# Optimization experiments

Measured on AMD Instinct MI355X. Metric: run time of the kernel, lower is better.

Reference implementation:

```python
import jax, jax.numpy as jnp
import numpy as np

T, B, D, H = 256, 64, 1024, 1024


def setup_inputs() -> dict:
    key = jax.random.key(0)
    ks = jax.random.split(key, 12)
    stdv = 1.0 / np.sqrt(H)
    u = lambda k, shape: jax.random.uniform(k, shape, jnp.float32, -stdv, stdv)
    return {
        "input_": jax.random.normal(ks[0], (T, B, D), jnp.float32),
        "length": jax.random.randint(ks[1], (B,), 1, T + 1, jnp.int32),
        "h0": jnp.zeros((B, H), jnp.float32),
        "cj": jax.random.normal(ks[2], (B, H), jnp.float32),
        "he": jax.random.normal(ks[3], (B, H), jnp.float32),
        "w_ih": u(ks[4], (3 * H, D)),
        "w_hh": u(ks[5], (3 * H, H)),
        "w_ch": u(ks[6], (3 * H, H)),
        "w_zh": u(ks[7], (3 * H, H)),
        "b_ih": u(ks[8], (3 * H,)),
        "b_hh": u(ks[9], (3 * H,)),
        "b_ch": u(ks[10], (3 * H,)),
        "b_zh": u(ks[11], (3 * H,)),
    }


def _chunk3(g):
    # mirrors torch .chunk(3, 1) on a (..., 3H) tensor
    return g[..., :H], g[..., H:2 * H], g[..., 2 * H:]


def reference(input_, length, h0, cj, he, w_ih, w_hh, w_ch, w_zh,
              b_ih, b_hh, b_ch, b_zh):
    # context projections are time-invariant: hoist out of the recurrence
    c_r, c_i, c_n = _chunk3(cj @ w_ch.T + b_ch)   # (B,H) each
    z_r, z_i, z_n = _chunk3(he @ w_zh.T + b_zh)   # (B,H) each
    # input projections for all steps at once: (T,B,3H)
    gi_all = jnp.einsum('tbd,gd->tbg', input_, w_ih) + b_ih

    def step(h, xs):
        gi_t, t = xs
        i_r, i_i, i_n = _chunk3(gi_t)
        h_r, h_i, h_n_ = _chunk3(h @ w_hh.T + b_hh)
        resetgate = jax.nn.sigmoid(i_r + h_r + c_r + z_r)
        inputgate = jax.nn.sigmoid(i_i + h_i + c_i + z_i)
        newgate = jnp.tanh(i_n + resetgate * h_n_ + c_n + z_n)
        hy = newgate + inputgate * (h - newgate)
        mask = (t < length).astype(hy.dtype)[:, None]          # (B,1)
        # NOTE: faithful to original torch code, which uses hx[0]
        # (first batch row, broadcast) in the masked branch.
        h_next = hy * mask + h[0] * (1.0 - mask)
        return h_next, h_next

    h_last, output = jax.lax.scan(step, h0, (gi_all, jnp.arange(T)))
    h_n = h_last[None]  # (num_layers=1, B, H)
    return output, h_n
```

## Files before the change

### kernel.cpp

```cpp
#include <hip/hip_runtime.h>
#include <stdint.h>

#define TT 256
#define BB 64
#define DD 1024
#define HH 1024
#define G3 3072

typedef unsigned long long ull;
typedef __attribute__((ext_vector_type(8))) short short8;
typedef __attribute__((ext_vector_type(4))) float f32x4;

__device__ __forceinline__ unsigned short f2bf(float f) {
  union { float f; unsigned int i; } v; v.f = f;
  unsigned int x = v.i;
  return (unsigned short)((x + 0x7fffu + ((x >> 16) & 1u)) >> 16);
}
__device__ __forceinline__ float bf2f(unsigned short u) {
  union { unsigned int i; float f; } v; v.i = ((unsigned int)u) << 16; return v.f;
}
__device__ __forceinline__ f32x4 mfma16(short8 a, short8 b, f32x4 c) {
  return __builtin_amdgcn_mfma_f32_16x16x32_bf16(a, b, c, 0, 0, 0);
}
__device__ __forceinline__ void gload_lds16(const void* g, void* l) {
  __builtin_amdgcn_global_load_lds((const __attribute__((address_space(1))) void*)g,
                                   (__attribute__((address_space(3))) void*)l,
                                   16, 0, 0);
}

__global__ void k_cvt_bf16(const float* __restrict__ in, unsigned short* __restrict__ out, int n4) {
  int i = blockIdx.x * blockDim.x + threadIdx.x;
  int stride = gridDim.x * blockDim.x;
  for (; i < n4; i += stride) {
    float4 v = ((const float4*)in)[i];
    ushort4 o;
    o.x = f2bf(v.x); o.y = f2bf(v.y); o.z = f2bf(v.z); o.w = f2bf(v.w);
    ((ushort4*)out)[i] = o;
  }
}

__global__ __launch_bounds__(256) void k_ctx(
    const unsigned short* __restrict__ cjb, const unsigned short* __restrict__ heb,
    const unsigned short* __restrict__ Wchb, const unsigned short* __restrict__ Wzhb,
    const float* __restrict__ b_ih, const float* __restrict__ b_hh,
    const float* __restrict__ b_ch, const float* __restrict__ b_zh,
    float* __restrict__ E) {
  __shared__ f32x4 red[4][4][64];
  int n0 = blockIdx.x * 16;
  int tid = threadIdx.x;
  int w = tid >> 6, l = tid & 63, lo = l & 15, hi = l >> 4;
  f32x4 acc[4];
#pragma unroll
  for (int r = 0; r < 4; r++) acc[r] = (f32x4){0.f, 0.f, 0.f, 0.f};
#pragma unroll 4
  for (int kk = 0; kk < 16; kk++) {
    int k = w * 512 + kk * 32;
    const unsigned short* Asrc = (k < 1024) ? cjb : heb;
    const unsigned short* Bsrc = (k < 1024) ? Wchb : Wzhb;
    int kw = (k < 1024) ? k : (k - 1024);
    int kof = kw + hi * 8;
    short8 bf = *(const short8*)(Bsrc + (size_t)(n0 + lo) * 1024 + kof);
#pragma unroll
    for (int r = 0; r < 4; r++) {
      short8 af = *(const short8*)(Asrc + (size_t)(r * 16 + lo) * 1024 + kof);
      acc[r] = mfma16(af, bf, acc[r]);
    }
  }
#pragma unroll
  for (int r = 0; r < 4; r++) red[w][r][l] = acc[r];
  __syncthreads();
  f32x4 s = red[0][w][l];
#pragma unroll
  for (int w2 = 1; w2 < 4; w2++) {
    f32x4 p = red[w2][w][l];
    s[0] += p[0]; s[1] += p[1]; s[2] += p[2]; s[3] += p[3];
  }
  int g = n0 + lo;
  float bias = b_ih[g] + b_ch[g] + b_zh[g] + ((g < 2048) ? b_hh[g] : 0.0f);
#pragma unroll
  for (int j = 0; j < 4; j++) {
    int b = w * 16 + hi * 4 + j;
    E[(size_t)b * G3 + g] = s[j] + bias;
  }
}

__global__ __launch_bounds__(256) void k_gemm_gi(
    const unsigned short* __restrict__ Xb,
    const unsigned short* __restrict__ Wb,
    const float* __restrict__ E,
    unsigned short* __restrict__ gi) {
  __shared__ unsigned short As[128 * 32];
  __shared__ unsigned short Bs[128 * 32];
  int bid = blockIdx.x;
  int mt = bid & 127;
  int nt = bid >> 7;
  int m0 = mt * 128, n0 = nt * 128;
  int tid = threadIdx.x;
  int w = tid >> 6, l = tid & 63, lo = l & 15, hi = l >> 4;
  int wr = w >> 1, wc = w & 1;
  f32x4 acc[4][4];
#pragma unroll
  for (int i = 0; i < 4; i++)
#pragma unroll
    for (int j = 0; j < 4; j++) acc[i][j] = (f32x4){0.f, 0.f, 0.f, 0.f};
  int srow = tid >> 2;
  int scol = (tid & 3) * 8;
  for (int kt = 0; kt < 32; kt++) {
    int k0 = kt * 32;
    __syncthreads();
    gload_lds16(Xb + (size_t)(m0 + srow) * 1024 + k0 + scol, As + srow * 32 + scol);
    gload_lds16(Xb + (size_t)(m0 + 64 + srow) * 1024 + k0 + scol, As + (64 + srow) * 32 + scol);
    gload_lds16(Wb + (size_t)(n0 + srow) * 1024 + k0 + scol, Bs + srow * 32 + scol);
    gload_lds16(Wb + (size_t)(n0 + 64 + srow) * 1024 + k0 + scol, Bs + (64 + srow) * 32 + scol);
    asm volatile("s_waitcnt vmcnt(0)" ::: "memory");
    __syncthreads();
    short8 a[4], b[4];
#pragma unroll
    for (int i = 0; i < 4; i++) a[i] = *(const short8*)(As + (wr * 64 + i * 16 + lo) * 32 + hi * 8);
#pragma unroll
    for (int i = 0; i < 4; i++) b[i] = *(const short8*)(Bs + (wc * 64 + i * 16 + lo) * 32 + hi * 8);
#pragma unroll
    for (int i = 0; i < 4; i++)
#pragma unroll
      for (int j = 0; j < 4; j++) acc[i][j] = mfma16(a[i], b[j], acc[i][j]);
  }
#pragma unroll
  for (int i = 0; i < 4; i++)
#pragma unroll
    for (int j = 0; j < 4; j++)
#pragma unroll
      for (int e = 0; e < 4; e++) {
        int r = m0 + wr * 64 + i * 16 + hi * 4 + e;
        int c = n0 + wc * 64 + j * 16 + lo;
        float v = acc[i][j][e] + E[(size_t)(r & 63) * G3 + c];
        gi[(size_t)r * G3 + c] = f2bf(v);
      }
}

__global__ __launch_bounds__(256) void k_rnn(
    const unsigned short* __restrict__ giE,
    const unsigned short* __restrict__ Whhb,
    const float* __restrict__ b_hh,
    const float* __restrict__ h0,
    const int* __restrict__ length,
    unsigned short* __restrict__ hbuf,
    float* __restrict__ out,
    float* __restrict__ hn,
    unsigned int* __restrict__ seq) {
  extern __shared__ char smem[];
  unsigned short* wlds = (unsigned short*)smem;
  f32x4* red = (f32x4*)(smem + 98304);
  float* hp0 = (float*)(smem + 98304 + 49152);

  const int cs = blockIdx.x;
  const int j0 = cs * 16;
  const int tid = threadIdx.x;
  const int kq = tid >> 6, l = tid & 63, lo = l & 15, hi = l >> 4;
  const int rowbase = kq * 16;
  const int col = j0 + lo;

#pragma unroll
  for (int kk = 0; kk < 8; ++kk)
#pragma unroll
    for (int s = 0; s < 3; ++s) {
      int f = (kq * 8 + kk) * 3 + s;
      short8 v = *(const short8*)(Whhb + (size_t)(s * 1024 + j0 + lo) * 1024 + kq * 256 + kk * 32 + hi * 8);
      ((short8*)wlds)[f * 64 + l] = v;
    }

  const float bhhn = b_hh[2048 + col];
  float hown[4];
  int len4[4];
#pragma unroll
  for (int j = 0; j < 4; ++j) {
    int b = rowbase + hi * 4 + j;
    hown[j] = h0[(size_t)b * 1024 + col];
    len4[j] = length[b];
  }
#pragma unroll
  for (int j = 0; j < 4; ++j) {
    unsigned int mine = f2bf(hown[j]);
    unsigned int oth = __shfl_xor(mine, 1, 64);
    if (!(lo & 1)) {
      int row = rowbase + hi * 4 + j;
      __hip_atomic_store((unsigned int*)(hbuf + (size_t)cs * 1024 + row * 16 + lo),
                         mine | (oth << 16), __ATOMIC_RELAXED, __HIP_MEMORY_SCOPE_AGENT);
    }
  }
  if (kq == 0 && hi == 0) hp0[lo] = hown[0];
  float gir[3][4];
#pragma unroll
  for (int s = 0; s < 3; ++s)
#pragma unroll
    for (int j = 0; j < 4; ++j)
      gir[s][j] = bf2f(giE[(size_t)(rowbase + hi * 4 + j) * G3 + s * 1024 + col]);
  __syncthreads();
  asm volatile("s_waitcnt vmcnt(0)" ::: "memory");
  if (l == 0)
    __hip_atomic_store(&seq[(cs * 4 + kq) * 16], 1u, __ATOMIC_RELAXED, __HIP_MEMORY_SCOPE_AGENT);

  int slot = 0;
  for (int t = 0; t < TT; ++t) {
    const int nslot = (slot == 2) ? 0 : slot + 1;
    {
      const unsigned int* sp = seq + ((size_t)(kq * 16 + (l >> 2)) * 4 + (l & 3)) * 16;
      unsigned int tgt = (unsigned int)(t + 1);
      for (;;) {
        unsigned int v = __hip_atomic_load(sp, __ATOMIC_RELAXED, __HIP_MEMORY_SCOPE_AGENT);
        if (__all(v >= tgt)) break;
        __builtin_amdgcn_s_sleep(1);
      }
    }
    const unsigned short* hb2 = hbuf + (size_t)slot * 65536;
    union AF { ull u[2]; short8 v; };
    AF a[4][8];
#pragma unroll
    for (int rt = 0; rt < 4; ++rt)
#pragma unroll
      for (int kk = 0; kk < 8; ++kk) {
        int k = kq * 256 + kk * 32;
        int blk = (k >> 4) + (hi >> 1);
        const unsigned short* hp = hb2 + (size_t)blk * 1024 + (rt * 16 + lo) * 16 + (hi & 1) * 8;
        a[rt][kk].u[0] = __hip_atomic_load((const ull*)hp, __ATOMIC_RELAXED, __HIP_MEMORY_SCOPE_AGENT);
        a[rt][kk].u[1] = __hip_atomic_load((const ull*)hp + 1, __ATOMIC_RELAXED, __HIP_MEMORY_SCOPE_AGENT);
      }
    f32x4 acc[4][3];
#pragma unroll
    for (int rt = 0; rt < 4; ++rt)
#pragma unroll
      for (int s = 0; s < 3; ++s) acc[rt][s] = (f32x4){0.f, 0.f, 0.f, 0.f};
#pragma unroll
    for (int kk = 0; kk < 8; ++kk) {
      const short8* wf = ((const short8*)wlds) + (size_t)((kq * 8 + kk) * 3) * 64 + l;
      short8 b0 = wf[0];
      short8 b1 = wf[64];
      short8 b2 = wf[128];
#pragma unroll
      for (int rt = 0; rt < 4; ++rt) {
        acc[rt][0] = mfma16(a[rt][kk].v, b0, acc[rt][0]);
        acc[rt][1] = mfma16(a[rt][kk].v, b1, acc[rt][1]);
        acc[rt][2] = mfma16(a[rt][kk].v, b2, acc[rt][2]);
      }
    }
#pragma unroll
    for (int rt = 0; rt < 4; ++rt)
#pragma unroll
      for (int s = 0; s < 3; ++s)
        red[((size_t)kq * 12 + rt * 3 + s) * 64 + l] = acc[rt][s];
    __syncthreads();
    f32x4 fin[3];
#pragma unroll
    for (int s = 0; s < 3; ++s) {
      f32x4 v = red[((size_t)0 * 12 + kq * 3 + s) * 64 + l];
#pragma unroll
      for (int q = 1; q < 4; ++q) {
        f32x4 p = red[((size_t)q * 12 + kq * 3 + s) * 64 + l];
        v[0] += p[0]; v[1] += p[1]; v[2] += p[2]; v[3] += p[3];
      }
      fin[s] = v;
    }
    float h0p = hp0[(t & 1) * 16 + lo];
    __syncthreads();
    float hv[4];
#pragma unroll
    for (int j = 0; j < 4; ++j) {
      float R = fin[0][j] + gir[0][j];
      float I = fin[1][j] + gir[1][j];
      float rg = 1.f / (1.f + __expf(-R));
      float ig = 1.f / (1.f + __expf(-I));
      float nx = gir[2][j] + rg * (fin[2][j] + bhhn);
      nx = fminf(15.f, fmaxf(-15.f, nx));
      float e2 = __expf(2.f * nx);
      float ng = (e2 - 1.f) / (e2 + 1.f);
      float hy = ng + ig * (hown[j] - ng);
      float res = (t < len4[j]) ? hy : h0p;
      hv[j] = res;
      hown[j] = res;
    }
    if (t < TT - 1) {
      unsigned short* dst = hbuf + (size_t)nslot * 65536 + (size_t)cs * 1024;
#pragma unroll
      for (int j = 0; j < 4; ++j) {
        unsigned int mine = f2bf(hv[j]);
        unsigned int oth = __shfl_xor(mine, 1, 64);
        if (!(lo & 1)) {
          int row = rowbase + hi * 4 + j;
          __hip_atomic_store((unsigned int*)(dst + row * 16 + lo),
                             mine | (oth << 16), __ATOMIC_RELAXED, __HIP_MEMORY_SCOPE_AGENT);
        }
      }
      if (kq == 0 && hi == 0) hp0[((t + 1) & 1) * 16 + lo] = hv[0];
      asm volatile("s_waitcnt vmcnt(0)" ::: "memory");
      if (l == 0)
        __hip_atomic_store(&seq[(cs * 4 + kq) * 16], (unsigned int)(t + 2),
                           __ATOMIC_RELAXED, __HIP_MEMORY_SCOPE_AGENT);
    }
#pragma unroll
    for (int j = 0; j < 4; ++j) {
      int b = rowbase + hi * 4 + j;
      out[(size_t)t * (BB * HH) + (size_t)b * 1024 + col] = hv[j];
    }
    if (t == TT - 1) {
#pragma unroll
      for (int j = 0; j < 4; ++j) {
        int b = rowbase + hi * 4 + j;
        hn[(size_t)b * 1024 + col] = hv[j];
      }
    } else {
      const unsigned short* gb = giE + (size_t)(t + 1) * 64 * G3;
#pragma unroll
      for (int s = 0; s < 3; ++s)
#pragma unroll
        for (int j = 0; j < 4; ++j)
          gir[s][j] = bf2f(gb[(size_t)(rowbase + hi * 4 + j) * G3 + s * 1024 + col]);
    }
    slot = nslot;
  }
}

extern "C" void kernel_launch(void* const* d_in, const int* in_sizes, int n_in,
                              void* d_out, int out_size, void* d_ws, size_t ws_size,
                              hipStream_t stream) {
  const float* input_ = (const float*)d_in[0];
  const int* length   = (const int*)d_in[1];
  const float* h0     = (const float*)d_in[2];
  const float* cj     = (const float*)d_in[3];
  const float* he     = (const float*)d_in[4];
  const float* w_ih   = (const float*)d_in[5];
  const float* w_hh   = (const float*)d_in[6];
  const float* w_ch   = (const float*)d_in[7];
  const float* w_zh   = (const float*)d_in[8];
  const float* b_ih   = (const float*)d_in[9];
  const float* b_hh   = (const float*)d_in[10];
  const float* b_ch   = (const float*)d_in[11];
  const float* b_zh   = (const float*)d_in[12];

  char* ws = (char*)d_ws;
  const size_t OFF_SEQ   = 0;
  const size_t OFF_XB    = 131072;
  const size_t OFF_WIHB  = OFF_XB + 33554432ull;
  const size_t OFF_WHHB  = OFF_WIHB + 6291456ull;
  const size_t OFF_WCHB  = OFF_WHHB + 6291456ull;
  const size_t OFF_WZHB  = OFF_WCHB + 6291456ull;
  const size_t OFF_CJB   = OFF_WZHB + 6291456ull;
  const size_t OFF_HEB   = OFF_CJB + 131072ull;
  const size_t OFF_E     = OFF_HEB + 131072ull;
  const size_t OFF_GI    = OFF_E + 786432ull;
  const size_t OFF_HBUF  = OFF_GI + 100663296ull;

  unsigned int* seq     = (unsigned int*)(ws + OFF_SEQ);
  unsigned short* Xb    = (unsigned short*)(ws + OFF_XB);
  unsigned short* Wihb  = (unsigned short*)(ws + OFF_WIHB);
  unsigned short* Whhb  = (unsigned short*)(ws + OFF_WHHB);
  unsigned short* Wchb  = (unsigned short*)(ws + OFF_WCHB);
  unsigned short* Wzhb  = (unsigned short*)(ws + OFF_WZHB);
  unsigned short* cjb   = (unsigned short*)(ws + OFF_CJB);
  unsigned short* heb   = (unsigned short*)(ws + OFF_HEB);
  float* E              = (float*)(ws + OFF_E);
  unsigned short* gi    = (unsigned short*)(ws + OFF_GI);
  unsigned short* hbuf  = (unsigned short*)(ws + OFF_HBUF);

  float* out = (float*)d_out;
  float* hn  = out + 16777216;

  hipFuncSetAttribute((const void*)k_rnn, hipFuncAttributeMaxDynamicSharedMemorySize, 147584);

  hipMemsetAsync(seq, 0, 16384, stream);
  k_cvt_bf16<<<2048, 256, 0, stream>>>(input_, Xb, 16777216 / 4);
  k_cvt_bf16<<<1024, 256, 0, stream>>>(w_ih, Wihb, 3145728 / 4);
  k_cvt_bf16<<<1024, 256, 0, stream>>>(w_hh, Whhb, 3145728 / 4);
  k_cvt_bf16<<<1024, 256, 0, stream>>>(w_ch, Wchb, 3145728 / 4);
  k_cvt_bf16<<<1024, 256, 0, stream>>>(w_zh, Wzhb, 3145728 / 4);
  k_cvt_bf16<<<64, 256, 0, stream>>>(cj, cjb, 65536 / 4);
  k_cvt_bf16<<<64, 256, 0, stream>>>(he, heb, 65536 / 4);
  k_ctx<<<192, 256, 0, stream>>>(cjb, heb, Wchb, Wzhb, b_ih, b_hh, b_ch, b_zh, E);
  k_gemm_gi<<<3072, 256, 0, stream>>>(Xb, Wihb, E, gi);
  k_rnn<<<64, 256, 147584, stream>>>(gi, Whhb, b_hh, h0, length, hbuf, out, hn, seq);
}
```

Baseline: 1.454 ms.

## Split recurrent GEMM by batch rows across two waves instead of K-split reduction

The recurrent kernel drops to 128 threads per block, with each wave owning 32 batch rows over the full K dimension. This removes the LDS cross-wave reduction and its two block barriers per step. Hidden-state loads become explicit cache-bypassing dwordx4 loads issued in four software-pipelined chunks with manual vmcnt waits. The buffer goes from triple to double, and the gate inputs are held as bf16 in registers. This lengthens each wave's serial MFMA chain and raises register pressure, and relies on the flag protocol staying safe with only two buffers.

```diff
diff --git a/kernel.cpp b/kernel.cpp
--- a/kernel.cpp
+++ b/kernel.cpp
@@ -26,6 +26,11 @@
   __builtin_amdgcn_global_load_lds((const __attribute__((address_space(1))) void*)g,
                                    (__attribute__((address_space(3))) void*)l,
                                    16, 0, 0);
+}
+__device__ __forceinline__ short8 mall_load16(const unsigned short* p) {
+  short8 r;
+  asm volatile("global_load_dwordx4 %0, %1, off sc0 sc1" : "=v"(r) : "v"(p));
+  return r;
 }
 
 __global__ void k_cvt_bf16(const float* __restrict__ in, unsigned short* __restrict__ out, int n4) {
@@ -137,7 +142,7 @@
       }
 }
 
-__global__ __launch_bounds__(256) void k_rnn(
+__global__ __launch_bounds__(128) void k_rnn(
     const unsigned short* __restrict__ giE,
     const unsigned short* __restrict__ Whhb,
     const float* __restrict__ b_hh,
@@ -149,173 +154,193 @@
     unsigned int* __restrict__ seq) {
   extern __shared__ char smem[];
   unsigned short* wlds = (unsigned short*)smem;
-  f32x4* red = (f32x4*)(smem + 98304);
-  float* hp0 = (float*)(smem + 98304 + 49152);
-
-  const int cs = blockIdx.x;
-  const int j0 = cs * 16;
+  float* h0f = (float*)(smem + 98304);
+
+  const int cs = blockIdx.x, j0 = cs * 16;
   const int tid = threadIdx.x;
-  const int kq = tid >> 6, l = tid & 63, lo = l & 15, hi = l >> 4;
-  const int rowbase = kq * 16;
+  const int w = tid >> 6, l = tid & 63, lo = l & 15, hi = l >> 4;
+  const int rowbase = w * 32;
   const int col = j0 + lo;
 
 #pragma unroll
-  for (int kk = 0; kk < 8; ++kk)
+  for (int k2 = 0; k2 < 16; ++k2) {
+    int kk = w * 16 + k2;
 #pragma unroll
     for (int s = 0; s < 3; ++s) {
-      int f = (kq * 8 + kk) * 3 + s;
-      short8 v = *(const short8*)(Whhb + (size_t)(s * 1024 + j0 + lo) * 1024 + kq * 256 + kk * 32 + hi * 8);
+      int f = kk * 3 + s;
+      short8 v = *(const short8*)(Whhb + (size_t)(s * 1024 + j0 + lo) * 1024 + kk * 32 + hi * 8);
       ((short8*)wlds)[f * 64 + l] = v;
     }
-
+  }
   const float bhhn = b_hh[2048 + col];
-  float hown[4];
-  int len4[4];
+  float hA[4], hB[4];
+  int lenA[4], lenB[4];
 #pragma unroll
   for (int j = 0; j < 4; ++j) {
-    int b = rowbase + hi * 4 + j;
-    hown[j] = h0[(size_t)b * 1024 + col];
-    len4[j] = length[b];
-  }
-#pragma unroll
-  for (int j = 0; j < 4; ++j) {
-    unsigned int mine = f2bf(hown[j]);
-    unsigned int oth = __shfl_xor(mine, 1, 64);
-    if (!(lo & 1)) {
-      int row = rowbase + hi * 4 + j;
-      __hip_atomic_store((unsigned int*)(hbuf + (size_t)cs * 1024 + row * 16 + lo),
-                         mine | (oth << 16), __ATOMIC_RELAXED, __HIP_MEMORY_SCOPE_AGENT);
-    }
-  }
-  if (kq == 0 && hi == 0) hp0[lo] = hown[0];
-  float gir[3][4];
-#pragma unroll
-  for (int s = 0; s < 3; ++s)
-#pragma unroll
-    for (int j = 0; j < 4; ++j)
-      gir[s][j] = bf2f(giE[(size_t)(rowbase + hi * 4 + j) * G3 + s * 1024 + col]);
+    int rA = rowbase + hi * 4 + j, rB = rA + 16;
+    hA[j] = h0[(size_t)rA * 1024 + col]; lenA[j] = length[rA];
+    hB[j] = h0[(size_t)rB * 1024 + col]; lenB[j] = length[rB];
+  }
+  {
+    unsigned short* dst = hbuf + (size_t)cs * 1024;
+#pragma unroll
+    for (int j = 0; j < 4; ++j) {
+      unsigned int mA = f2bf(hA[j]), mB = f2bf(hB[j]);
+      unsigned int oA = __shfl_xor(mA, 1, 64), oB = __shfl_xor(mB, 1, 64);
+      if (!(lo & 1)) {
+        int rr = rowbase + hi * 4 + j;
+        __hip_atomic_store((unsigned int*)(dst + rr * 16 + lo), mA | (oA << 16),
+                           __ATOMIC_RELAXED, __HIP_MEMORY_SCOPE_AGENT);
+        __hip_atomic_store((unsigned int*)(dst + (rr + 16) * 16 + lo), mB | (oB << 16),
+                           __ATOMIC_RELAXED, __HIP_MEMORY_SCOPE_AGENT);
+      }
+    }
+  }
+  if (w == 0 && hi == 0) h0f[lo] = hA[0];
   __syncthreads();
   asm volatile("s_waitcnt vmcnt(0)" ::: "memory");
   if (l == 0)
-    __hip_atomic_store(&seq[(cs * 4 + kq) * 16], 1u, __ATOMIC_RELAXED, __HIP_MEMORY_SCOPE_AGENT);
-
-  int slot = 0;
+    __hip_atomic_store(&seq[(cs * 2 + w) * 16], 1u, __ATOMIC_RELAXED, __HIP_MEMORY_SCOPE_AGENT);
+  unsigned short gir[24];
+#pragma unroll
+  for (int r2 = 0; r2 < 2; ++r2)
+#pragma unroll
+    for (int s = 0; s < 3; ++s)
+#pragma unroll
+      for (int j = 0; j < 4; ++j)
+        gir[(r2 * 3 + s) * 4 + j] =
+            giE[(size_t)(rowbase + r2 * 16 + hi * 4 + j) * G3 + s * 1024 + col];
+
+#define ISSUE(c, X)                                                                    \
+  _Pragma("unroll") for (int k2 = 0; k2 < 8; ++k2) {                                   \
+    int kk = (c) * 8 + k2;                                                             \
+    size_t cb = (size_t)(kk * 2 + (hi >> 1));                                          \
+    X[k2 * 2 + 0] = mall_load16(base + (cb * 64 + rowbase + lo) * 16 + (hi & 1) * 8);  \
+    X[k2 * 2 + 1] = mall_load16(base + (cb * 64 + rowbase + 16 + lo) * 16 + (hi & 1) * 8); \
+  }
+#define WAITV(N)                                                                       \
+  asm volatile("s_waitcnt vmcnt(" #N ")" ::: "memory");                                \
+  __builtin_amdgcn_sched_barrier(0)
+#define CRUNCH(c, X)                                                                   \
+  _Pragma("unroll") for (int k2 = 0; k2 < 8; ++k2) {                                   \
+    int kk = (c) * 8 + k2;                                                             \
+    const short8* wf = ((const short8*)wlds) + (size_t)(kk * 3) * 64 + l;              \
+    short8 b0 = wf[0], b1 = wf[64], b2 = wf[128];                                      \
+    a00 = mfma16(X[k2 * 2 + 0], b0, a00);                                              \
+    a01 = mfma16(X[k2 * 2 + 0], b1, a01);                                              \
+    a02 = mfma16(X[k2 * 2 + 0], b2, a02);                                              \
+    a10 = mfma16(X[k2 * 2 + 1], b0, a10);                                              \
+    a11 = mfma16(X[k2 * 2 + 1], b1, a11);                                              \
+    a12 = mfma16(X[k2 * 2 + 1], b2, a12);                                              \
+  }
+
   for (int t = 0; t < TT; ++t) {
-    const int nslot = (slot == 2) ? 0 : slot + 1;
     {
-      const unsigned int* sp = seq + ((size_t)(kq * 16 + (l >> 2)) * 4 + (l & 3)) * 16;
+      const unsigned int* sp0 = seq + (size_t)(2 * l) * 16;
+      const unsigned int* sp1 = sp0 + 16;
       unsigned int tgt = (unsigned int)(t + 1);
       for (;;) {
-        unsigned int v = __hip_atomic_load(sp, __ATOMIC_RELAXED, __HIP_MEMORY_SCOPE_AGENT);
-        if (__all(v >= tgt)) break;
+        unsigned int v0 = __hip_atomic_load(sp0, __ATOMIC_RELAXED, __HIP_MEMORY_SCOPE_AGENT);
+        unsigned int v1 = __hip_atomic_load(sp1, __ATOMIC_RELAXED, __HIP_MEMORY_SCOPE_AGENT);
+        if (__all((v0 >= tgt) && (v1 >= tgt))) break;
         __builtin_amdgcn_s_sleep(1);
       }
     }
-    const unsigned short* hb2 = hbuf + (size_t)slot * 65536;
-    union AF { ull u[2]; short8 v; };
-    AF a[4][8];
-#pragma unroll
-    for (int rt = 0; rt < 4; ++rt)
-#pragma unroll
-      for (int kk = 0; kk < 8; ++kk) {
-        int k = kq * 256 + kk * 32;
-        int blk = (k >> 4) + (hi >> 1);
-        const unsigned short* hp = hb2 + (size_t)blk * 1024 + (rt * 16 + lo) * 16 + (hi & 1) * 8;
-        a[rt][kk].u[0] = __hip_atomic_load((const ull*)hp, __ATOMIC_RELAXED, __HIP_MEMORY_SCOPE_AGENT);
-        a[rt][kk].u[1] = __hip_atomic_load((const ull*)hp + 1, __ATOMIC_RELAXED, __HIP_MEMORY_SCOPE_AGENT);
-      }
-    f32x4 acc[4][3];
-#pragma unroll
-    for (int rt = 0; rt < 4; ++rt)
-#pragma unroll
-      for (int s = 0; s < 3; ++s) acc[rt][s] = (f32x4){0.f, 0.f, 0.f, 0.f};
-#pragma unroll
-    for (int kk = 0; kk < 8; ++kk) {
-      const short8* wf = ((const short8*)wlds) + (size_t)((kq * 8 + kk) * 3) * 64 + l;
-      short8 b0 = wf[0];
-      short8 b1 = wf[64];
-      short8 b2 = wf[128];
-#pragma unroll
-      for (int rt = 0; rt < 4; ++rt) {
-        acc[rt][0] = mfma16(a[rt][kk].v, b0, acc[rt][0]);
-        acc[rt][1] = mfma16(a[rt][kk].v, b1, acc[rt][1]);
-        acc[rt][2] = mfma16(a[rt][kk].v, b2, acc[rt][2]);
-      }
-    }
-#pragma unroll
-    for (int rt = 0; rt < 4; ++rt)
-#pragma unroll
-      for (int s = 0; s < 3; ++s)
-        red[((size_t)kq * 12 + rt * 3 + s) * 64 + l] = acc[rt][s];
-    __syncthreads();
-    f32x4 fin[3];
-#pragma unroll
-    for (int s = 0; s < 3; ++s) {
-      f32x4 v = red[((size_t)0 * 12 + kq * 3 + s) * 64 + l];
-#pragma unroll
-      for (int q = 1; q < 4; ++q) {
-        f32x4 p = red[((size_t)q * 12 + kq * 3 + s) * 64 + l];
-        v[0] += p[0]; v[1] += p[1]; v[2] += p[2]; v[3] += p[3];
-      }
-      fin[s] = v;
-    }
-    float h0p = hp0[(t & 1) * 16 + lo];
-    __syncthreads();
-    float hv[4];
+    const unsigned short* base = hbuf + ((size_t)(t & 1) * 64) * 1024;
+    f32x4 a00 = {0.f, 0.f, 0.f, 0.f}, a01 = a00, a02 = a00, a10 = a00, a11 = a00, a12 = a00;
+    {
+      short8 XA[16], XB[16];
+      ISSUE(0, XA);
+      ISSUE(1, XB);
+      WAITV(16);
+      CRUNCH(0, XA);
+      ISSUE(2, XA);
+      WAITV(16);
+      CRUNCH(1, XB);
+      ISSUE(3, XB);
+      WAITV(16);
+      CRUNCH(2, XA);
+      WAITV(0);
+      CRUNCH(3, XB);
+    }
+    float h0p = (w == 0) ? __shfl(hA[0], lo, 64) : h0f[(t & 1) * 16 + lo];
+    float rA[4], rB[4];
 #pragma unroll
     for (int j = 0; j < 4; ++j) {
-      float R = fin[0][j] + gir[0][j];
-      float I = fin[1][j] + gir[1][j];
+      float R = a00[j] + bf2f(gir[0 * 4 + j]);
+      float I = a01[j] + bf2f(gir[1 * 4 + j]);
       float rg = 1.f / (1.f + __expf(-R));
       float ig = 1.f / (1.f + __expf(-I));
-      float nx = gir[2][j] + rg * (fin[2][j] + bhhn);
+      float nx = bf2f(gir[2 * 4 + j]) + rg * (a02[j] + bhhn);
       nx = fminf(15.f, fmaxf(-15.f, nx));
       float e2 = __expf(2.f * nx);
       float ng = (e2 - 1.f) / (e2 + 1.f);
-      float hy = ng + ig * (hown[j] - ng);
-      float res = (t < len4[j]) ? hy : h0p;
-      hv[j] = res;
-      hown[j] = res;
-    }
+      float hy = ng + ig * (hA[j] - ng);
+      rA[j] = (t < lenA[j]) ? hy : h0p;
+    }
+#pragma unroll
+    for (int j = 0; j < 4; ++j) {
+      float R = a10[j] + bf2f(gir[(3 + 0) * 4 + j]);
+      float I = a11[j] + bf2f(gir[(3 + 1) * 4 + j]);
+      float rg = 1.f / (1.f + __expf(-R));
+      float ig = 1.f / (1.f + __expf(-I));
+      float nx = bf2f(gir[(3 + 2) * 4 + j]) + rg * (a12[j] + bhhn);
+      nx = fminf(15.f, fmaxf(-15.f, nx));
+      float e2 = __expf(2.f * nx);
+      float ng = (e2 - 1.f) / (e2 + 1.f);
+      float hy = ng + ig * (hB[j] - ng);
+      rB[j] = (t < lenB[j]) ? hy : h0p;
+    }
+#pragma unroll
+    for (int j = 0; j < 4; ++j) { hA[j] = rA[j]; hB[j] = rB[j]; }
     if (t < TT - 1) {
-      unsigned short* dst = hbuf + (size_t)nslot * 65536 + (size_t)cs * 1024;
+      unsigned short* dst = hbuf + ((size_t)((t + 1) & 1) * 64 + cs) * 1024;
 #pragma unroll
       for (int j = 0; j < 4; ++j) {
-        unsigned int mine = f2bf(hv[j]);
-        unsigned int oth = __shfl_xor(mine, 1, 64);
+        unsigned int mA = f2bf(hA[j]), mB = f2bf(hB[j]);
+        unsigned int oA = __shfl_xor(mA, 1, 64), oB = __shfl_xor(mB, 1, 64);
         if (!(lo & 1)) {
-          int row = rowbase + hi * 4 + j;
-          __hip_atomic_store((unsigned int*)(dst + row * 16 + lo),
-                             mine | (oth << 16), __ATOMIC_RELAXED, __HIP_MEMORY_SCOPE_AGENT);
+          int rr = rowbase + hi * 4 + j;
+          __hip_atomic_store((unsigned int*)(dst + rr * 16 + lo), mA | (oA << 16),
+                             __ATOMIC_RELAXED, __HIP_MEMORY_SCOPE_AGENT);
+          __hip_atomic_store((unsigned int*)(dst + (rr + 16) * 16 + lo), mB | (oB << 16),
+                             __ATOMIC_RELAXED, __HIP_MEMORY_SCOPE_AGENT);
         }
       }
-      if (kq == 0 && hi == 0) hp0[((t + 1) & 1) * 16 + lo] = hv[0];
-      asm volatile("s_waitcnt vmcnt(0)" ::: "memory");
+      if (w == 0 && hi == 0) h0f[((t + 1) & 1) * 16 + lo] = hA[0];
+      asm volatile("s_waitcnt vmcnt(0) lgkmcnt(0)" ::: "memory");
       if (l == 0)
-        __hip_atomic_store(&seq[(cs * 4 + kq) * 16], (unsigned int)(t + 2),
+        __hip_atomic_store(&seq[(cs * 2 + w) * 16], (unsigned int)(t + 2),
                            __ATOMIC_RELAXED, __HIP_MEMORY_SCOPE_AGENT);
-    }
-#pragma unroll
-    for (int j = 0; j < 4; ++j) {
-      int b = rowbase + hi * 4 + j;
-      out[(size_t)t * (BB * HH) + (size_t)b * 1024 + col] = hv[j];
-    }
-    if (t == TT - 1) {
 #pragma unroll
       for (int j = 0; j < 4; ++j) {
-        int b = rowbase + hi * 4 + j;
-        hn[(size_t)b * 1024 + col] = hv[j];
-      }
+        int rr = rowbase + hi * 4 + j;
+        out[(size_t)t * (BB * HH) + (size_t)rr * 1024 + col] = rA[j];
+        out[(size_t)t * (BB * HH) + (size_t)(rr + 16) * 1024 + col] = rB[j];
+      }
+      const unsigned short* gb = giE + (size_t)(t + 1) * 64 * G3;
+#pragma unroll
+      for (int r2 = 0; r2 < 2; ++r2)
+#pragma unroll
+        for (int s = 0; s < 3; ++s)
+#pragma unroll
+          for (int j = 0; j < 4; ++j)
+            gir[(r2 * 3 + s) * 4 + j] =
+                gb[(size_t)(rowbase + r2 * 16 + hi * 4 + j) * G3 + s * 1024 + col];
     } else {
-      const unsigned short* gb = giE + (size_t)(t + 1) * 64 * G3;
-#pragma unroll
-      for (int s = 0; s < 3; ++s)
-#pragma unroll
-        for (int j = 0; j < 4; ++j)
-          gir[s][j] = bf2f(gb[(size_t)(rowbase + hi * 4 + j) * G3 + s * 1024 + col]);
-    }
-    slot = nslot;
-  }
+#pragma unroll
+      for (int j = 0; j < 4; ++j) {
+        int rr = rowbase + hi * 4 + j;
+        out[(size_t)t * (BB * HH) + (size_t)rr * 1024 + col] = rA[j];
+        out[(size_t)t * (BB * HH) + (size_t)(rr + 16) * 1024 + col] = rB[j];
+        hn[(size_t)rr * 1024 + col] = rA[j];
+        hn[(size_t)(rr + 16) * 1024 + col] = rB[j];
+      }
+    }
+  }
+#undef ISSUE
+#undef WAITV
+#undef CRUNCH
 }
 
 extern "C" void kernel_launch(void* const* d_in, const int* in_sizes, int n_in,
@@ -337,7 +362,8 @@
 
   char* ws = (char*)d_ws;
   const size_t OFF_SEQ   = 0;
-  const size_t OFF_XB    = 131072;
+  const size_t OFF_HBUF  = 16384;
+  const size_t OFF_XB    = 524288;
   const size_t OFF_WIHB  = OFF_XB + 33554432ull;
   const size_t OFF_WHHB  = OFF_WIHB + 6291456ull;
   const size_t OFF_WCHB  = OFF_WHHB + 6291456ull;
@@ -346,9 +372,9 @@
   const size_t OFF_HEB   = OFF_CJB + 131072ull;
   const size_t OFF_E     = OFF_HEB + 131072ull;
   const size_t OFF_GI    = OFF_E + 786432ull;
-  const size_t OFF_HBUF  = OFF_GI + 100663296ull;
 
   unsigned int* seq     = (unsigned int*)(ws + OFF_SEQ);
+  unsigned short* hbuf  = (unsigned short*)(ws + OFF_HBUF);
   unsigned short* Xb    = (unsigned short*)(ws + OFF_XB);
   unsigned short* Wihb  = (unsigned short*)(ws + OFF_WIHB);
   unsigned short* Whhb  = (unsigned short*)(ws + OFF_WHHB);
@@ -358,12 +384,11 @@
   unsigned short* heb   = (unsigned short*)(ws + OFF_HEB);
   float* E              = (float*)(ws + OFF_E);
   unsigned short* gi    = (unsigned short*)(ws + OFF_GI);
-  unsigned short* hbuf  = (unsigned short*)(ws + OFF_HBUF);
 
   float* out = (float*)d_out;
   float* hn  = out + 16777216;
 
-  hipFuncSetAttribute((const void*)k_rnn, hipFuncAttributeMaxDynamicSharedMemorySize, 147584);
+  hipFuncSetAttribute((const void*)k_rnn, hipFuncAttributeMaxDynamicSharedMemorySize, 98432);
 
   hipMemsetAsync(seq, 0, 16384, stream);
   k_cvt_bf16<<<2048, 256, 0, stream>>>(input_, Xb, 16777216 / 4);
@@ -375,5 +400,5 @@
   k_cvt_bf16<<<64, 256, 0, stream>>>(he, heb, 65536 / 4);
   k_ctx<<<192, 256, 0, stream>>>(cjb, heb, Wchb, Wzhb, b_ih, b_hh, b_ch, b_zh, E);
   k_gemm_gi<<<3072, 256, 0, stream>>>(Xb, Wihb, E, gi);
-  k_rnn<<<64, 256, 147584, stream>>>(gi, Whhb, b_hh, h0, length, hbuf, out, hn, seq);
-}
+  k_rnn<<<64, 128, 98432, stream>>>(gi, Whhb, b_hh, h0, length, hbuf, out, hn, seq);
+}
```

Result: faster. 1.408 ms, median of 2 (-3.2%).
